# Performance work log

Hardware: AMD Instinct MI355X
Metric: run time of the kernel (lower is better)

The kernel has to match this reference:

```python
import jax, jax.numpy as jnp
import numpy as np

B, S = 2048, 256
V, E, H, LAT, NL = 4, 8, 64, 3, 2
NT = V + 2          # vocab + start + pad tokens
START = V
TEMP = 1.0


def setup_inputs() -> dict:
    key = jax.random.key(0)
    ks = jax.random.split(key, 32)
    def p(k, shape, scale=0.1):
        return jax.random.normal(k, shape, jnp.float32) * scale
    return {
        "tokens": jax.random.randint(ks[0], (B, S), 0, V),
        "emb": p(ks[1], (NT, E)),
        "enc_Wih0": p(ks[2], (3 * H, E)), "enc_Whh0": p(ks[3], (3 * H, H)),
        "enc_bih0": p(ks[4], (3 * H,)), "enc_bhh0": p(ks[5], (3 * H,)),
        "enc_Wih1": p(ks[6], (3 * H, H)), "enc_Whh1": p(ks[7], (3 * H, H)),
        "enc_bih1": p(ks[8], (3 * H,)), "enc_bhh1": p(ks[9], (3 * H,)),
        "fc_mu_W": p(ks[10], (LAT, H)), "fc_mu_b": p(ks[11], (LAT,)),
        "fc_var_W": p(ks[12], (LAT, H)), "fc_var_b": p(ks[13], (LAT,)),
        "dec_emb": p(ks[14], (NT, H)),
        "proj_W": p(ks[15], (H, LAT)), "proj_b": p(ks[16], (H,)),
        "dec_Wih0": p(ks[17], (3 * H, H)), "dec_Whh0": p(ks[18], (3 * H, H)),
        "dec_bih0": p(ks[19], (3 * H,)), "dec_bhh0": p(ks[20], (3 * H,)),
        "dec_Wih1": p(ks[21], (3 * H, H)), "dec_Whh1": p(ks[22], (3 * H, H)),
        "dec_bih1": p(ks[23], (3 * H,)), "dec_bhh1": p(ks[24], (3 * H,)),
        "head_W": p(ks[25], (V, H)), "head_b": p(ks[26], (V,)),
    }


def gru_cell(h, x, Wih, Whh, bih, bhh):
    # PyTorch GRU gate order: reset, update, new
    gi = x @ Wih.T + bih            # [B, 3H]
    gh = h @ Whh.T + bhh            # [B, 3H]
    ir, iz, ig = jnp.split(gi, 3, axis=-1)
    hr, hz, hg = jnp.split(gh, 3, axis=-1)
    r = jax.nn.sigmoid(ir + hr)
    z = jax.nn.sigmoid(iz + hz)
    n = jnp.tanh(ig + r * hg)
    return (1.0 - z) * n + z * h


def run_gru_layer(x, Wih, Whh, bih, bhh):
    # x: [B, S, D] -> (outputs [B, S, H], final hidden [B, H])
    def step(h, xt):
        h2 = gru_cell(h, xt, Wih, Whh, bih, bhh)
        return h2, h2
    h0 = jnp.zeros((x.shape[0], Whh.shape[1]), x.dtype)
    hT, ys = jax.lax.scan(step, h0, x.transpose(1, 0, 2))
    return ys.transpose(1, 0, 2), hT


def reference(tokens, emb, enc_Wih0, enc_Whh0, enc_bih0, enc_bhh0,
              enc_Wih1, enc_Whh1, enc_bih1, enc_bhh1,
              fc_mu_W, fc_mu_b, fc_var_W, fc_var_b,
              dec_emb, proj_W, proj_b,
              dec_Wih0, dec_Whh0, dec_bih0, dec_bhh0,
              dec_Wih1, dec_Whh1, dec_bih1, dec_bhh1,
              head_W, head_b):
    b, s = tokens.shape
    # ---- encode ----
    x = emb[tokens]                                   # [B, S, E]
    seq, _ = run_gru_layer(x, enc_Wih0, enc_Whh0, enc_bih0, enc_bhh0)
    _, h_last = run_gru_layer(seq, enc_Wih1, enc_Whh1, enc_bih1, enc_bhh1)
    mu = h_last @ fc_mu_W.T + fc_mu_b                 # [B, LAT]
    log_var = h_last @ fc_var_W.T + fc_var_b          # [B, LAT]
    # ---- reparameterize ----
    eps = jax.random.normal(jax.random.key(1), mu.shape, mu.dtype)
    z = eps * jnp.exp(0.5 * log_var) + mu
    hz = z @ proj_W.T + proj_b                        # [B, H]; same init for both layers
    tok0 = jnp.full((b,), START, jnp.int32)
    keys = jax.random.split(jax.random.key(2), s)
    def step(carry, k):
        h0, h1, tok = carry
        xe = dec_emb[tok]                             # [B, H]
        h0n = gru_cell(h0, xe, dec_Wih0, dec_Whh0, dec_bih0, dec_bhh0)
        h1n = gru_cell(h1, h0n, dec_Wih1, dec_Whh1, dec_bih1, dec_bhh1)
        logits = (h1n @ head_W.T + head_b) / TEMP     # [B, V]
        probs = jax.nn.softmax(logits, axis=-1)
        nt = jax.random.categorical(k, logits)        # multinomial sample (detached)
        return (h0n, h1n, nt), probs
    _, probs_seq = jax.lax.scan(step, (hz, hz, tok0), keys)   # [S, B, V]
    recons = probs_seq.transpose(1, 0, 2)[:, :, None, :]      # [B, S, 1, V]
    return recons, tokens, mu, log_var
```

## Files before the change

### kernel.cpp

```cpp
#include <hip/hip_runtime.h>
#include <stdint.h>

typedef unsigned int u32;
typedef unsigned short u16;

#define NB   2048
#define SS   256
#define HH   64
#define VV   4
#define LATD 3
#define NTHR 512

#define TOK_OFF (NB*SS*VV)
#define MU_OFF  (TOK_OFF + NB*SS)
#define LV_OFF  (MU_OFF + NB*LATD)

__device__ __forceinline__ void tf2x32(u32 k0, u32 k1, u32 x0, u32 x1, u32& o0, u32& o1){
  u32 k2 = k0 ^ k1 ^ 0x1BD11BDAu;
  x0 += k0; x1 += k1;
#define TFR(r) { x0 += x1; x1 = (x1<<r)|(x1>>(32-r)); x1 ^= x0; }
  TFR(13) TFR(15) TFR(26) TFR(6)   x0 += k1; x1 += k2 + 1u;
  TFR(17) TFR(29) TFR(16) TFR(24)  x0 += k2; x1 += k0 + 2u;
  TFR(13) TFR(15) TFR(26) TFR(6)   x0 += k0; x1 += k1 + 3u;
  TFR(17) TFR(29) TFR(16) TFR(24)  x0 += k1; x1 += k2 + 4u;
  TFR(13) TFR(15) TFR(26) TFR(6)   x0 += k2; x1 += k0 + 5u;
#undef TFR
  o0 = x0; o1 = x1;
}
__device__ __forceinline__ u32 foldb(u32 k0, u32 k1, u32 i){
  u32 a,b; tf2x32(k0,k1,0u,i,a,b); return a^b;
}
__device__ __forceinline__ float b2u(u32 bits){
  union{u32 i;float f;}c; c.i = (bits>>9) | 0x3f800000u; return c.f - 1.0f;
}
__device__ __forceinline__ float erfinv_f(float x){
  float w = -log1pf(-x*x);
  float p;
  if (w < 5.0f){
    w -= 2.5f;
    p = 2.81022636e-08f;
    p = fmaf(p,w, 3.43273939e-07f);
    p = fmaf(p,w,-3.5233877e-06f);
    p = fmaf(p,w,-4.39150654e-06f);
    p = fmaf(p,w, 0.00021858087f);
    p = fmaf(p,w,-0.00125372503f);
    p = fmaf(p,w,-0.00417768164f);
    p = fmaf(p,w, 0.246640727f);
    p = fmaf(p,w, 1.50140941f);
  } else {
    w = sqrtf(w) - 3.0f;
    p = -0.000200214257f;
    p = fmaf(p,w, 0.000100950558f);
    p = fmaf(p,w, 0.00134934322f);
    p = fmaf(p,w,-0.00367342844f);
    p = fmaf(p,w, 0.00573950773f);
    p = fmaf(p,w,-0.0076224613f);
    p = fmaf(p,w, 0.00943887047f);
    p = fmaf(p,w, 1.00167406f);
    p = fmaf(p,w, 2.83297682f);
  }
  return p*x;
}
__device__ __forceinline__ float sigm(float x){ return 1.0f/(1.0f+expf(-x)); }
__device__ __forceinline__ float rl(float x, int l){
  return __int_as_float(__builtin_amdgcn_readlane(__float_as_int(x), l));
}
__device__ __forceinline__ float wred(float x){
  #pragma unroll
  for (int m=1; m<64; m<<=1) x += __shfl_xor(x, m, 64);
  return x;
}

#define MATVEC1R(Wr, Wz, Wn, xv, ar, az, an)                                   \
  _Pragma("unroll")                                                            \
  for (int k4 = 0; k4 < 16; k4++){                                             \
    float4 wr = Wr[k4];                                                        \
    float4 wz = Wz[k4];                                                        \
    float4 wn = Wn[k4];                                                        \
    float x0 = rl(xv, 4*k4), x1 = rl(xv, 4*k4+1), x2 = rl(xv, 4*k4+2), x3 = rl(xv, 4*k4+3); \
    ar = fmaf(wr.x,x0,ar); ar = fmaf(wr.y,x1,ar); ar = fmaf(wr.z,x2,ar); ar = fmaf(wr.w,x3,ar); \
    az = fmaf(wz.x,x0,az); az = fmaf(wz.y,x1,az); az = fmaf(wz.z,x2,az); az = fmaf(wz.w,x3,az); \
    an = fmaf(wn.x,x0,an); an = fmaf(wn.y,x1,an); an = fmaf(wn.z,x2,an); an = fmaf(wn.w,x3,an); \
  }

#define MATVEC1L(W, xv, ar, az, an)                                            \
  _Pragma("unroll 2")                                                          \
  for (int k4 = 0; k4 < 16; k4++){                                             \
    float4 wr = W[k4*192 + j];                                                 \
    float4 wz = W[k4*192 + 64 + j];                                            \
    float4 wn = W[k4*192 + 128 + j];                                           \
    float x0 = rl(xv, 4*k4), x1 = rl(xv, 4*k4+1), x2 = rl(xv, 4*k4+2), x3 = rl(xv, 4*k4+3); \
    ar = fmaf(wr.x,x0,ar); ar = fmaf(wr.y,x1,ar); ar = fmaf(wr.z,x2,ar); ar = fmaf(wr.w,x3,ar); \
    az = fmaf(wz.x,x0,az); az = fmaf(wz.y,x1,az); az = fmaf(wz.z,x2,az); az = fmaf(wz.w,x3,az); \
    an = fmaf(wn.x,x0,an); an = fmaf(wn.y,x1,an); an = fmaf(wn.z,x2,an); an = fmaf(wn.w,x3,an); \
  }

#define LOAD_REG_W(G, Ar, Az, An)                                              \
  _Pragma("unroll")                                                            \
  for (int k4 = 0; k4 < 16; k4++){                                             \
    Ar[k4] = G[(j)*16 + k4];                                                   \
    Az[k4] = G[(64 + j)*16 + k4];                                              \
    An[k4] = G[(128 + j)*16 + k4];                                             \
  }

#define PIN4(v) asm volatile("" : "+v"(v.x), "+v"(v.y), "+v"(v.z), "+v"(v.w))
#define PIN_W(Ar, Az, An)                                                      \
  _Pragma("unroll")                                                            \
  for (int k4 = 0; k4 < 16; k4++){ PIN4(Ar[k4]); PIN4(Az[k4]); PIN4(An[k4]); }

__global__ __launch_bounds__(NTHR, 2) void enc_kernel(
    const int* __restrict__ tokens, const float* __restrict__ emb,
    const float* __restrict__ Wih0, const float* __restrict__ Whh0,
    const float* __restrict__ bih0, const float* __restrict__ bhh0,
    const float* __restrict__ Wih1, const float* __restrict__ Whh1,
    const float* __restrict__ bih1, const float* __restrict__ bhh1,
    const float* __restrict__ muW, const float* __restrict__ mub,
    const float* __restrict__ vaW, const float* __restrict__ vab,
    const float* __restrict__ pW,  const float* __restrict__ pb,
    float* __restrict__ out, float* __restrict__ hz_ws)
{
  __shared__ float4 wi1[16*192];
  __shared__ float4 wh1[16*192];
  __shared__ float tokT[VV*192];

  const int tid = threadIdx.x;
  const int b0  = blockIdx.x * 8;
  const int j   = tid & 63;
  const int wv  = tid >> 6;
  const int row = b0 + wv;

  for (int i4 = tid; i4 < 3072; i4 += NTHR){
    int g = i4 >> 4, k4 = i4 & 15;
    wi1[k4*192 + g] = ((const float4*)Wih1)[i4];
    wh1[k4*192 + g] = ((const float4*)Whh1)[i4];
  }
  if (tid < 192){
    #pragma unroll
    for (int v = 0; v < VV; v++){
      float acc = 0.0f;
      #pragma unroll
      for (int e = 0; e < 8; e++) acc = fmaf(emb[v*8+e], Wih0[tid*8+e], acc);
      tokT[v*192 + tid] = acc + bih0[tid];
    }
  }
  for (int i = tid; i < 8*SS; i += NTHR){
    int rr = i >> 8, tq = i & 255;
    out[TOK_OFF + (b0+rr)*SS + tq] = (float)tokens[(b0+rr)*SS + tq];
  }

  float4 w0r[16], w0z[16], w0n[16];
  {
    const float4* G0 = (const float4*)Whh0;
    LOAD_REG_W(G0, w0r, w0z, w0n)
    PIN_W(w0r, w0z, w0n)
  }
  __syncthreads();

  const float bhr0 = bhh0[j], bhz0 = bhh0[64+j], bhn0 = bhh0[128+j];
  const float bir1 = bih1[j], biz1 = bih1[64+j], bin1 = bih1[128+j];
  const float bhr1 = bhh1[j], bhz1 = bhh1[64+j], bhn1 = bhh1[128+j];

  float h0 = 0.0f, h1 = 0.0f;
  const int tR = row*SS;

  for (int t = 0; t < SS; t++){
    asm volatile("" ::: "memory");
    int k = tokens[tR + t];
    float ar=0, az=0, an=0;
    MATVEC1R(w0r, w0z, w0n, h0, ar, az, an)
    {
      float ir = tokT[k*192+j], iz = tokT[k*192+64+j], ig = tokT[k*192+128+j];
      float rg = sigm(ir + ar + bhr0);
      float zg = sigm(iz + az + bhz0);
      float ng = tanhf(ig + rg*(an + bhn0));
      h0 = (1.0f - zg)*ng + zg*h0;
    }
    float air=0, aiz=0, ain=0, ahr=0, ahz=0, ahn=0;
    MATVEC1L(wi1, h0, air, aiz, ain)
    MATVEC1L(wh1, h1, ahr, ahz, ahn)
    {
      float rg = sigm(air + bir1 + ahr + bhr1);
      float zg = sigm(aiz + biz1 + ahz + bhz1);
      float ng = tanhf(ain + bin1 + rg*(ahn + bhn1));
      h1 = (1.0f - zg)*ng + zg*h1;
    }
  }

  const float LO_ = -0.99999994f;
  {
    float hv = h1;
    int gb = row;
    float mu0,mu1,mu2, lv0,lv1,lv2;
    { float pm = muW[0*64+j]*hv; pm = wred(pm); mu0 = pm + mub[0];
      float pv = vaW[0*64+j]*hv; pv = wred(pv); lv0 = pv + vab[0]; }
    { float pm = muW[1*64+j]*hv; pm = wred(pm); mu1 = pm + mub[1];
      float pv = vaW[1*64+j]*hv; pv = wred(pv); lv1 = pv + vab[1]; }
    { float pm = muW[2*64+j]*hv; pm = wred(pm); mu2 = pm + mub[2];
      float pv = vaW[2*64+j]*hv; pv = wred(pv); lv2 = pv + vab[2]; }
    if (j < 3){
      float mv  = (j==0)?mu0:(j==1)?mu1:mu2;
      float lvv = (j==0)?lv0:(j==1)?lv1:lv2;
      out[MU_OFF + gb*LATD + j] = mv;
      out[LV_OFF + gb*LATD + j] = lvv;
    }
    float z0,z1,z2;
    #pragma unroll
    for (int l = 0; l < 3; l++){
      u32 bits = foldb(0u, 1u, (u32)(gb*LATD + l));
      float u01 = b2u(bits);
      float uu = u01 * 2.0f;
      uu = uu + LO_;
      uu = fmaxf(LO_, uu);
      float ep = 1.41421354f * erfinv_f(uu);
      float lvv = (l==0)?lv0:(l==1)?lv1:lv2;
      float mvv = (l==0)?mu0:(l==1)?mu1:mu2;
      float zv = ep * expf(0.5f*lvv) + mvv;
      if (l==0) z0 = zv; else if (l==1) z1 = zv; else z2 = zv;
    }
    float hzj = pW[j*3+0]*z0;
    hzj += pW[j*3+1]*z1;
    hzj += pW[j*3+2]*z2;
    hzj += pb[j];
    hz_ws[gb*HH + j] = hzj;
  }
}

__global__ __launch_bounds__(NTHR, 2) void dec_kernel(
    const float* __restrict__ demb,
    const float* __restrict__ Wih0, const float* __restrict__ Whh0,
    const float* __restrict__ bih0, const float* __restrict__ bhh0,
    const float* __restrict__ Wih1, const float* __restrict__ Whh1,
    const float* __restrict__ bih1, const float* __restrict__ bhh1,
    const float* __restrict__ headW, const float* __restrict__ headb,
    const float* __restrict__ hz_ws, float* __restrict__ out)
{
  __shared__ float4 wi1[16*192];
  __shared__ float4 wh1[16*192];
  __shared__ float decT[6*192];
  __shared__ u32 sk0[SS], sk1[SS];
  __shared__ float gmbT[8][SS*VV];

  const int tid = threadIdx.x;
  const int b0  = blockIdx.x * 8;
  const int j   = tid & 63;
  const int wv  = tid >> 6;
  const int row = b0 + wv;

  for (int i4 = tid; i4 < 3072; i4 += NTHR){
    int g = i4 >> 4, k4 = i4 & 15;
    wi1[k4*192 + g] = ((const float4*)Wih1)[i4];
    wh1[k4*192 + g] = ((const float4*)Whh1)[i4];
  }
  if (tid < 192){
    #pragma unroll
    for (int v = 0; v < 6; v++){
      float acc = 0.0f;
      #pragma unroll 8
      for (int k = 0; k < 64; k++) acc = fmaf(demb[v*64+k], Wih0[tid*64+k], acc);
      decT[v*192 + tid] = acc + bih0[tid];
    }
  }
  if (tid < SS){
    u32 a,b; tf2x32(0u, 2u, 0u, (u32)tid, a, b);
    sk0[tid] = a; sk1[tid] = b;
  }

  float4 w0r[16], w0z[16], w0n[16];
  {
    const float4* G0 = (const float4*)Whh0;
    LOAD_REG_W(G0, w0r, w0z, w0n)
  }
  __syncthreads();

  const float TINY = 1.17549435e-38f;
  for (int idx = j; idx < SS*VV; idx += 64){
    int t = idx >> 2, v = idx & 3;
    u32 bits = foldb(sk0[t], sk1[t], (u32)(row*VV + v));
    float u01 = b2u(bits);
    float u = u01 + TINY;
    u = fmaxf(TINY, u);
    gmbT[wv][idx] = -logf(-logf(u));
  }

  const float bhr0 = bhh0[j], bhz0 = bhh0[64+j], bhn0 = bhh0[128+j];
  const float bir1 = bih1[j], biz1 = bih1[64+j], bin1 = bih1[128+j];
  const float bhr1 = bhh1[j], bhz1 = bhh1[64+j], bhn1 = bhh1[128+j];
  const float hw0 = headW[0*64+j], hw1 = headW[1*64+j], hw2 = headW[2*64+j], hw3 = headW[3*64+j];
  const float hb0 = headb[0], hb1 = headb[1], hb2 = headb[2], hb3 = headb[3];

  float h0 = hz_ws[row*HH + j];
  float h1 = h0;
  int tk = 4;

  const int vv = j & 3;

  float ar=0, az=0, an=0;
  MATVEC1R(w0r, w0z, w0n, h0, ar, az, an)
  float ahr=0, ahz=0, ahn=0;
  MATVEC1L(wh1, h1, ahr, ahz, ahn)

  for (int t = 0; t < SS; t++){
    asm volatile("" ::: "memory");
    {
      float ir = decT[tk*192+j], iz = decT[tk*192+64+j], ig = decT[tk*192+128+j];
      float rg = sigm(ir + ar + bhr0);
      float zg = sigm(iz + az + bhz0);
      float ng = tanhf(ig + rg*(an + bhn0));
      h0 = (1.0f - zg)*ng + zg*h0;
    }
    float air=0, aiz=0, ain=0;
    MATVEC1L(wi1, h0, air, aiz, ain)
    {
      float rg = sigm(air + bir1 + ahr + bhr1);
      float zg = sigm(aiz + biz1 + ahz + bhz1);
      float ng = tanhf(ain + bin1 + rg*(ahn + bhn1));
      h1 = (1.0f - zg)*ng + zg*h1;
    }
    float gmb = gmbT[wv][t*VV + vv];
    ar = 0.0f; az = 0.0f; an = 0.0f;
    MATVEC1R(w0r, w0z, w0n, h0, ar, az, an)
    ahr = 0.0f; ahz = 0.0f; ahn = 0.0f;
    MATVEC1L(wh1, h1, ahr, ahz, ahn)
    float l0 = wred(hw0*h1) + hb0;
    float l1 = wred(hw1*h1) + hb1;
    float l2 = wred(hw2*h1) + hb2;
    float l3 = wred(hw3*h1) + hb3;
    float lg = (vv==0)?l0:(vv==1)?l1:(vv==2)?l2:l3;
    float prt = lg + gmb;
    float mx = lg;
    mx = fmaxf(mx, __shfl_xor(mx, 1, 64));
    mx = fmaxf(mx, __shfl_xor(mx, 2, 64));
    float e = expf(lg - mx);
    float se = e;
    se += __shfl_xor(se, 1, 64);
    se += __shfl_xor(se, 2, 64);
    float prob = e / se;
    float bp = prt; int bv = vv;
    { float o = __shfl_xor(bp, 1, 64); int ov = __shfl_xor(bv, 1, 64);
      if (o > bp || (o == bp && ov < bv)){ bp = o; bv = ov; } }
    { float o = __shfl_xor(bp, 2, 64); int ov = __shfl_xor(bv, 2, 64);
      if (o > bp || (o == bp && ov < bv)){ bp = o; bv = ov; } }
    if (j < 4) out[(size_t)row*SS*VV + (size_t)t*VV + vv] = prob;
    tk = __builtin_amdgcn_readlane(bv, 0);
  }
}

extern "C" void kernel_launch(void* const* d_in, const int* in_sizes, int n_in,
                              void* d_out, int out_size, void* d_ws, size_t ws_size,
                              hipStream_t stream){
  const int*   tokens = (const int*)d_in[0];
  const float* emb    = (const float*)d_in[1];
  const float* eWih0  = (const float*)d_in[2];  const float* eWhh0 = (const float*)d_in[3];
  const float* ebih0  = (const float*)d_in[4];  const float* ebhh0 = (const float*)d_in[5];
  const float* eWih1  = (const float*)d_in[6];  const float* eWhh1 = (const float*)d_in[7];
  const float* ebih1  = (const float*)d_in[8];  const float* ebhh1 = (const float*)d_in[9];
  const float* muW    = (const float*)d_in[10]; const float* mub   = (const float*)d_in[11];
  const float* vaW    = (const float*)d_in[12]; const float* vab   = (const float*)d_in[13];
  const float* demb   = (const float*)d_in[14];
  const float* pW     = (const float*)d_in[15]; const float* pb    = (const float*)d_in[16];
  const float* dWih0  = (const float*)d_in[17]; const float* dWhh0 = (const float*)d_in[18];
  const float* dbih0  = (const float*)d_in[19]; const float* dbhh0 = (const float*)d_in[20];
  const float* dWih1  = (const float*)d_in[21]; const float* dWhh1 = (const float*)d_in[22];
  const float* dbih1  = (const float*)d_in[23]; const float* dbhh1 = (const float*)d_in[24];
  const float* hWp    = (const float*)d_in[25]; const float* hbp   = (const float*)d_in[26];
  float* out = (float*)d_out;
  float* hz = (float*)d_ws;

  enc_kernel<<<NB/8, NTHR, 0, stream>>>(tokens, emb,
      eWih0, eWhh0, ebih0, ebhh0, eWih1, eWhh1, ebih1, ebhh1,
      muW, mub, vaW, vab, pW, pb, out, hz);
  dec_kernel<<<NB/8, NTHR, 0, stream>>>(demb,
      dWih0, dWhh0, dbih0, dbhh0, dWih1, dWhh1, dbih1, dbhh1,
      hWp, hbp, hz, out);
}
```

Baseline: 2.560 ms.

## Fuse encoder and decoder into one kernel, keep latent in registers

Merges the encoder and decoder kernels into a single kernel, so the projected latent hz stays in a register instead of round-tripping through workspace memory, and one launch is removed. Shared memory for the layer-1 weights is reused between phases behind a barrier. The per-step Threefry key derivation moves inline into the Gumbel precompute. The four head logits are now reduced with a shared two-level shuffle tree instead of four full wave reductions. The merged kernel uses more shared memory, which may lower occupancy.

```diff
diff --git a/kernel.cpp b/kernel.cpp
--- a/kernel.cpp
+++ b/kernel.cpp
@@ -2,7 +2,6 @@
 #include <stdint.h>
 
 typedef unsigned int u32;
-typedef unsigned short u16;
 
 #define NB   2048
 #define SS   256
@@ -108,20 +107,28 @@
   _Pragma("unroll")                                                            \
   for (int k4 = 0; k4 < 16; k4++){ PIN4(Ar[k4]); PIN4(Az[k4]); PIN4(An[k4]); }
 
-__global__ __launch_bounds__(NTHR, 2) void enc_kernel(
+__global__ __launch_bounds__(NTHR, 2) void vae_kernel(
     const int* __restrict__ tokens, const float* __restrict__ emb,
-    const float* __restrict__ Wih0, const float* __restrict__ Whh0,
-    const float* __restrict__ bih0, const float* __restrict__ bhh0,
-    const float* __restrict__ Wih1, const float* __restrict__ Whh1,
-    const float* __restrict__ bih1, const float* __restrict__ bhh1,
+    const float* __restrict__ eWih0, const float* __restrict__ eWhh0,
+    const float* __restrict__ ebih0, const float* __restrict__ ebhh0,
+    const float* __restrict__ eWih1, const float* __restrict__ eWhh1,
+    const float* __restrict__ ebih1, const float* __restrict__ ebhh1,
     const float* __restrict__ muW, const float* __restrict__ mub,
     const float* __restrict__ vaW, const float* __restrict__ vab,
+    const float* __restrict__ demb,
     const float* __restrict__ pW,  const float* __restrict__ pb,
-    float* __restrict__ out, float* __restrict__ hz_ws)
+    const float* __restrict__ dWih0, const float* __restrict__ dWhh0,
+    const float* __restrict__ dbih0, const float* __restrict__ dbhh0,
+    const float* __restrict__ dWih1, const float* __restrict__ dWhh1,
+    const float* __restrict__ dbih1, const float* __restrict__ dbhh1,
+    const float* __restrict__ headW, const float* __restrict__ headb,
+    float* __restrict__ out)
 {
   __shared__ float4 wi1[16*192];
   __shared__ float4 wh1[16*192];
   __shared__ float tokT[VV*192];
+  __shared__ float decT[6*192];
+  __shared__ float gmbT[8][SS*VV];
 
   const int tid = threadIdx.x;
   const int b0  = blockIdx.x * 8;
@@ -129,65 +136,67 @@
   const int wv  = tid >> 6;
   const int row = b0 + wv;
 
-  for (int i4 = tid; i4 < 3072; i4 += NTHR){
-    int g = i4 >> 4, k4 = i4 & 15;
-    wi1[k4*192 + g] = ((const float4*)Wih1)[i4];
-    wh1[k4*192 + g] = ((const float4*)Whh1)[i4];
-  }
-  if (tid < 192){
-    #pragma unroll
-    for (int v = 0; v < VV; v++){
-      float acc = 0.0f;
+  float4 w0r[16], w0z[16], w0n[16];
+  float hzj;
+
+  {
+    for (int i4 = tid; i4 < 3072; i4 += NTHR){
+      int g = i4 >> 4, k4 = i4 & 15;
+      wi1[k4*192 + g] = ((const float4*)eWih1)[i4];
+      wh1[k4*192 + g] = ((const float4*)eWhh1)[i4];
+    }
+    if (tid < 192){
       #pragma unroll
-      for (int e = 0; e < 8; e++) acc = fmaf(emb[v*8+e], Wih0[tid*8+e], acc);
-      tokT[v*192 + tid] = acc + bih0[tid];
-    }
-  }
-  for (int i = tid; i < 8*SS; i += NTHR){
-    int rr = i >> 8, tq = i & 255;
-    out[TOK_OFF + (b0+rr)*SS + tq] = (float)tokens[(b0+rr)*SS + tq];
-  }
-
-  float4 w0r[16], w0z[16], w0n[16];
-  {
-    const float4* G0 = (const float4*)Whh0;
-    LOAD_REG_W(G0, w0r, w0z, w0n)
-    PIN_W(w0r, w0z, w0n)
-  }
-  __syncthreads();
-
-  const float bhr0 = bhh0[j], bhz0 = bhh0[64+j], bhn0 = bhh0[128+j];
-  const float bir1 = bih1[j], biz1 = bih1[64+j], bin1 = bih1[128+j];
-  const float bhr1 = bhh1[j], bhz1 = bhh1[64+j], bhn1 = bhh1[128+j];
-
-  float h0 = 0.0f, h1 = 0.0f;
-  const int tR = row*SS;
-
-  for (int t = 0; t < SS; t++){
-    asm volatile("" ::: "memory");
-    int k = tokens[tR + t];
-    float ar=0, az=0, an=0;
-    MATVEC1R(w0r, w0z, w0n, h0, ar, az, an)
+      for (int v = 0; v < VV; v++){
+        float acc = 0.0f;
+        #pragma unroll
+        for (int e = 0; e < 8; e++) acc = fmaf(emb[v*8+e], eWih0[tid*8+e], acc);
+        tokT[v*192 + tid] = acc + ebih0[tid];
+      }
+    }
+    for (int i = tid; i < 8*SS; i += NTHR){
+      int rr = i >> 8, tq = i & 255;
+      out[TOK_OFF + (b0+rr)*SS + tq] = (float)tokens[(b0+rr)*SS + tq];
+    }
+
     {
-      float ir = tokT[k*192+j], iz = tokT[k*192+64+j], ig = tokT[k*192+128+j];
-      float rg = sigm(ir + ar + bhr0);
-      float zg = sigm(iz + az + bhz0);
-      float ng = tanhf(ig + rg*(an + bhn0));
-      h0 = (1.0f - zg)*ng + zg*h0;
-    }
-    float air=0, aiz=0, ain=0, ahr=0, ahz=0, ahn=0;
-    MATVEC1L(wi1, h0, air, aiz, ain)
-    MATVEC1L(wh1, h1, ahr, ahz, ahn)
-    {
-      float rg = sigm(air + bir1 + ahr + bhr1);
-      float zg = sigm(aiz + biz1 + ahz + bhz1);
-      float ng = tanhf(ain + bin1 + rg*(ahn + bhn1));
-      h1 = (1.0f - zg)*ng + zg*h1;
-    }
-  }
-
-  const float LO_ = -0.99999994f;
-  {
+      const float4* G0 = (const float4*)eWhh0;
+      LOAD_REG_W(G0, w0r, w0z, w0n)
+      PIN_W(w0r, w0z, w0n)
+    }
+    __syncthreads();
+
+    const float bhr0 = ebhh0[j], bhz0 = ebhh0[64+j], bhn0 = ebhh0[128+j];
+    const float bir1 = ebih1[j], biz1 = ebih1[64+j], bin1 = ebih1[128+j];
+    const float bhr1 = ebhh1[j], bhz1 = ebhh1[64+j], bhn1 = ebhh1[128+j];
+
+    float h0 = 0.0f, h1 = 0.0f;
+    const int tR = row*SS;
+
+    for (int t = 0; t < SS; t++){
+      asm volatile("" ::: "memory");
+      int k = tokens[tR + t];
+      float ar=0, az=0, an=0;
+      MATVEC1R(w0r, w0z, w0n, h0, ar, az, an)
+      {
+        float ir = tokT[k*192+j], iz = tokT[k*192+64+j], ig = tokT[k*192+128+j];
+        float rg = sigm(ir + ar + bhr0);
+        float zg = sigm(iz + az + bhz0);
+        float ng = tanhf(ig + rg*(an + bhn0));
+        h0 = (1.0f - zg)*ng + zg*h0;
+      }
+      float air=0, aiz=0, ain=0, ahr=0, ahz=0, ahn=0;
+      MATVEC1L(wi1, h0, air, aiz, ain)
+      MATVEC1L(wh1, h1, ahr, ahz, ahn)
+      {
+        float rg = sigm(air + bir1 + ahr + bhr1);
+        float zg = sigm(aiz + biz1 + ahz + bhz1);
+        float ng = tanhf(ain + bin1 + rg*(ahn + bhn1));
+        h1 = (1.0f - zg)*ng + zg*h1;
+      }
+    }
+
+    const float LO_ = -0.99999994f;
     float hv = h1;
     int gb = row;
     float mu0,mu1,mu2, lv0,lv1,lv2;
@@ -217,131 +226,114 @@
       float zv = ep * expf(0.5f*lvv) + mvv;
       if (l==0) z0 = zv; else if (l==1) z1 = zv; else z2 = zv;
     }
-    float hzj = pW[j*3+0]*z0;
+    hzj = pW[j*3+0]*z0;
     hzj += pW[j*3+1]*z1;
     hzj += pW[j*3+2]*z2;
     hzj += pb[j];
-    hz_ws[gb*HH + j] = hzj;
-  }
-}
-
-__global__ __launch_bounds__(NTHR, 2) void dec_kernel(
-    const float* __restrict__ demb,
-    const float* __restrict__ Wih0, const float* __restrict__ Whh0,
-    const float* __restrict__ bih0, const float* __restrict__ bhh0,
-    const float* __restrict__ Wih1, const float* __restrict__ Whh1,
-    const float* __restrict__ bih1, const float* __restrict__ bhh1,
-    const float* __restrict__ headW, const float* __restrict__ headb,
-    const float* __restrict__ hz_ws, float* __restrict__ out)
-{
-  __shared__ float4 wi1[16*192];
-  __shared__ float4 wh1[16*192];
-  __shared__ float decT[6*192];
-  __shared__ u32 sk0[SS], sk1[SS];
-  __shared__ float gmbT[8][SS*VV];
-
-  const int tid = threadIdx.x;
-  const int b0  = blockIdx.x * 8;
-  const int j   = tid & 63;
-  const int wv  = tid >> 6;
-  const int row = b0 + wv;
-
+  }
+
+  __syncthreads();
   for (int i4 = tid; i4 < 3072; i4 += NTHR){
     int g = i4 >> 4, k4 = i4 & 15;
-    wi1[k4*192 + g] = ((const float4*)Wih1)[i4];
-    wh1[k4*192 + g] = ((const float4*)Whh1)[i4];
+    wi1[k4*192 + g] = ((const float4*)dWih1)[i4];
+    wh1[k4*192 + g] = ((const float4*)dWhh1)[i4];
   }
   if (tid < 192){
     #pragma unroll
     for (int v = 0; v < 6; v++){
       float acc = 0.0f;
       #pragma unroll 8
-      for (int k = 0; k < 64; k++) acc = fmaf(demb[v*64+k], Wih0[tid*64+k], acc);
-      decT[v*192 + tid] = acc + bih0[tid];
-    }
-  }
-  if (tid < SS){
-    u32 a,b; tf2x32(0u, 2u, 0u, (u32)tid, a, b);
-    sk0[tid] = a; sk1[tid] = b;
-  }
-
-  float4 w0r[16], w0z[16], w0n[16];
+      for (int k = 0; k < 64; k++) acc = fmaf(demb[v*64+k], dWih0[tid*64+k], acc);
+      decT[v*192 + tid] = acc + dbih0[tid];
+    }
+  }
   {
-    const float4* G0 = (const float4*)Whh0;
+    const float TINY = 1.17549435e-38f;
+    for (int idx = j; idx < SS*VV; idx += 64){
+      int t = idx >> 2, v = idx & 3;
+      u32 a,b; tf2x32(0u, 2u, 0u, (u32)t, a, b);
+      u32 bits = foldb(a, b, (u32)(row*VV + v));
+      float u01 = b2u(bits);
+      float u = u01 + TINY;
+      u = fmaxf(TINY, u);
+      gmbT[wv][idx] = -logf(-logf(u));
+    }
+  }
+  {
+    const float4* G0 = (const float4*)dWhh0;
     LOAD_REG_W(G0, w0r, w0z, w0n)
   }
   __syncthreads();
 
-  const float TINY = 1.17549435e-38f;
-  for (int idx = j; idx < SS*VV; idx += 64){
-    int t = idx >> 2, v = idx & 3;
-    u32 bits = foldb(sk0[t], sk1[t], (u32)(row*VV + v));
-    float u01 = b2u(bits);
-    float u = u01 + TINY;
-    u = fmaxf(TINY, u);
-    gmbT[wv][idx] = -logf(-logf(u));
-  }
-
-  const float bhr0 = bhh0[j], bhz0 = bhh0[64+j], bhn0 = bhh0[128+j];
-  const float bir1 = bih1[j], biz1 = bih1[64+j], bin1 = bih1[128+j];
-  const float bhr1 = bhh1[j], bhz1 = bhh1[64+j], bhn1 = bhh1[128+j];
-  const float hw0 = headW[0*64+j], hw1 = headW[1*64+j], hw2 = headW[2*64+j], hw3 = headW[3*64+j];
-  const float hb0 = headb[0], hb1 = headb[1], hb2 = headb[2], hb3 = headb[3];
-
-  float h0 = hz_ws[row*HH + j];
-  float h1 = h0;
-  int tk = 4;
-
-  const int vv = j & 3;
-
-  float ar=0, az=0, an=0;
-  MATVEC1R(w0r, w0z, w0n, h0, ar, az, an)
-  float ahr=0, ahz=0, ahn=0;
-  MATVEC1L(wh1, h1, ahr, ahz, ahn)
-
-  for (int t = 0; t < SS; t++){
-    asm volatile("" ::: "memory");
-    {
-      float ir = decT[tk*192+j], iz = decT[tk*192+64+j], ig = decT[tk*192+128+j];
-      float rg = sigm(ir + ar + bhr0);
-      float zg = sigm(iz + az + bhz0);
-      float ng = tanhf(ig + rg*(an + bhn0));
-      h0 = (1.0f - zg)*ng + zg*h0;
-    }
-    float air=0, aiz=0, ain=0;
-    MATVEC1L(wi1, h0, air, aiz, ain)
-    {
-      float rg = sigm(air + bir1 + ahr + bhr1);
-      float zg = sigm(aiz + biz1 + ahz + bhz1);
-      float ng = tanhf(ain + bin1 + rg*(ahn + bhn1));
-      h1 = (1.0f - zg)*ng + zg*h1;
-    }
-    float gmb = gmbT[wv][t*VV + vv];
-    ar = 0.0f; az = 0.0f; an = 0.0f;
+  {
+    const float bhr0 = dbhh0[j], bhz0 = dbhh0[64+j], bhn0 = dbhh0[128+j];
+    const float bir1 = dbih1[j], biz1 = dbih1[64+j], bin1 = dbih1[128+j];
+    const float bhr1 = dbhh1[j], bhz1 = dbhh1[64+j], bhn1 = dbhh1[128+j];
+    const float hw0 = headW[0*64+j], hw1 = headW[1*64+j], hw2 = headW[2*64+j], hw3 = headW[3*64+j];
+    const float hb0 = headb[0], hb1 = headb[1], hb2 = headb[2], hb3 = headb[3];
+
+    float h0 = hzj;
+    float h1 = h0;
+    int tk = 4;
+
+    const int vv = j & 3;
+    const float hbv = (vv==0)?hb0:(vv==1)?hb1:(vv==2)?hb2:hb3;
+
+    float ar=0, az=0, an=0;
     MATVEC1R(w0r, w0z, w0n, h0, ar, az, an)
-    ahr = 0.0f; ahz = 0.0f; ahn = 0.0f;
+    float ahr=0, ahz=0, ahn=0;
     MATVEC1L(wh1, h1, ahr, ahz, ahn)
-    float l0 = wred(hw0*h1) + hb0;
-    float l1 = wred(hw1*h1) + hb1;
-    float l2 = wred(hw2*h1) + hb2;
-    float l3 = wred(hw3*h1) + hb3;
-    float lg = (vv==0)?l0:(vv==1)?l1:(vv==2)?l2:l3;
-    float prt = lg + gmb;
-    float mx = lg;
-    mx = fmaxf(mx, __shfl_xor(mx, 1, 64));
-    mx = fmaxf(mx, __shfl_xor(mx, 2, 64));
-    float e = expf(lg - mx);
-    float se = e;
-    se += __shfl_xor(se, 1, 64);
-    se += __shfl_xor(se, 2, 64);
-    float prob = e / se;
-    float bp = prt; int bv = vv;
-    { float o = __shfl_xor(bp, 1, 64); int ov = __shfl_xor(bv, 1, 64);
-      if (o > bp || (o == bp && ov < bv)){ bp = o; bv = ov; } }
-    { float o = __shfl_xor(bp, 2, 64); int ov = __shfl_xor(bv, 2, 64);
-      if (o > bp || (o == bp && ov < bv)){ bp = o; bv = ov; } }
-    if (j < 4) out[(size_t)row*SS*VV + (size_t)t*VV + vv] = prob;
-    tk = __builtin_amdgcn_readlane(bv, 0);
+
+    for (int t = 0; t < SS; t++){
+      asm volatile("" ::: "memory");
+      {
+        float ir = decT[tk*192+j], iz = decT[tk*192+64+j], ig = decT[tk*192+128+j];
+        float rg = sigm(ir + ar + bhr0);
+        float zg = sigm(iz + az + bhz0);
+        float ng = tanhf(ig + rg*(an + bhn0));
+        h0 = (1.0f - zg)*ng + zg*h0;
+      }
+      float air=0, aiz=0, ain=0;
+      MATVEC1L(wi1, h0, air, aiz, ain)
+      {
+        float rg = sigm(air + bir1 + ahr + bhr1);
+        float zg = sigm(aiz + biz1 + ahz + bhz1);
+        float ng = tanhf(ain + bin1 + rg*(ahn + bhn1));
+        h1 = (1.0f - zg)*ng + zg*h1;
+      }
+      float gmb = gmbT[wv][t*VV + vv];
+      ar = 0.0f; az = 0.0f; an = 0.0f;
+      MATVEC1R(w0r, w0z, w0n, h0, ar, az, an)
+      ahr = 0.0f; ahz = 0.0f; ahn = 0.0f;
+      MATVEC1L(wh1, h1, ahr, ahz, ahn)
+      float p0 = hw0*h1, p1 = hw1*h1, p2 = hw2*h1, p3 = hw3*h1;
+      p0 += __shfl_xor(p0, 1, 64); p1 += __shfl_xor(p1, 1, 64);
+      p2 += __shfl_xor(p2, 1, 64); p3 += __shfl_xor(p3, 1, 64);
+      p0 += __shfl_xor(p0, 2, 64); p1 += __shfl_xor(p1, 2, 64);
+      p2 += __shfl_xor(p2, 2, 64); p3 += __shfl_xor(p3, 2, 64);
+      float lq = (vv==0)?p0:(vv==1)?p1:(vv==2)?p2:p3;
+      lq += __shfl_xor(lq, 4, 64);
+      lq += __shfl_xor(lq, 8, 64);
+      lq += __shfl_xor(lq, 16, 64);
+      lq += __shfl_xor(lq, 32, 64);
+      float lg = lq + hbv;
+      float prt = lg + gmb;
+      float mx = lg;
+      mx = fmaxf(mx, __shfl_xor(mx, 1, 64));
+      mx = fmaxf(mx, __shfl_xor(mx, 2, 64));
+      float e = expf(lg - mx);
+      float se = e;
+      se += __shfl_xor(se, 1, 64);
+      se += __shfl_xor(se, 2, 64);
+      float prob = e / se;
+      float bp = prt; int bv = vv;
+      { float o = __shfl_xor(bp, 1, 64); int ov = __shfl_xor(bv, 1, 64);
+        if (o > bp || (o == bp && ov < bv)){ bp = o; bv = ov; } }
+      { float o = __shfl_xor(bp, 2, 64); int ov = __shfl_xor(bv, 2, 64);
+        if (o > bp || (o == bp && ov < bv)){ bp = o; bv = ov; } }
+      if (j < 4) out[(size_t)row*SS*VV + (size_t)t*VV + vv] = prob;
+      tk = __builtin_amdgcn_readlane(bv, 0);
+    }
   }
 }
 
@@ -364,12 +356,11 @@
   const float* dbih1  = (const float*)d_in[23]; const float* dbhh1 = (const float*)d_in[24];
   const float* hWp    = (const float*)d_in[25]; const float* hbp   = (const float*)d_in[26];
   float* out = (float*)d_out;
-  float* hz = (float*)d_ws;
-
-  enc_kernel<<<NB/8, NTHR, 0, stream>>>(tokens, emb,
+  (void)d_ws; (void)ws_size;
+
+  vae_kernel<<<NB/8, NTHR, 0, stream>>>(tokens, emb,
       eWih0, eWhh0, ebih0, ebhh0, eWih1, eWhh1, ebih1, ebhh1,
-      muW, mub, vaW, vab, pW, pb, out, hz);
-  dec_kernel<<<NB/8, NTHR, 0, stream>>>(demb,
+      muW, mub, vaW, vab, demb, pW, pb,
       dWih0, dWhh0, dbih0, dbhh0, dWih1, dWhh1, dbih1, dbhh1,
-      hWp, hbp, hz, out);
-}
+      hWp, hbp, out);
+}
```

Result: no change. 2.577 ms (+0.6%).
